# Kernel optimization log

Measured on AMD Instinct MI355X. Metric: run time of the kernel, lower is better.

Reference implementation:

```python
import jax, jax.numpy as jnp
import numpy as np
import math

V = 200000      # num_symbols (pad idx = V)
D = 256         # embed_dim
B = 2048        # query batch
F = 5           # support (few-shot) size
N = 64          # max neighbors per entity
K = 32          # knn_k top-k neighbors kept by cosine sim
DM = 2 * D      # d_model of support/query encoders (512)
HID = 2 * DM    # LSTMCell hidden (1024)
STEPS = 4       # process_steps


def setup_inputs() -> dict:
    key = jax.random.key(0)
    ks = jax.random.split(key, 32)
    xav = lambda k, shp: jax.random.normal(k, shp, jnp.float32) * math.sqrt(2.0 / (shp[0] + shp[1]))
    u = 1.0 / math.sqrt(HID)
    inp = {
        # forward args (int indices)
        "query": jax.random.randint(ks[0], (B, 2), 0, V),
        "support": jax.random.randint(ks[1], (F, 2), 0, V),
        "q_l_conn": jax.random.randint(ks[2], (B, N, 2), 0, V),
        "q_l_deg": jax.random.randint(ks[3], (B,), 1, N),
        "q_r_conn": jax.random.randint(ks[4], (B, N, 2), 0, V),
        "q_r_deg": jax.random.randint(ks[5], (B,), 1, N),
        "s_l_conn": jax.random.randint(ks[6], (F, N, 2), 0, V),
        "s_l_deg": jax.random.randint(ks[7], (F,), 1, N),
        "s_r_conn": jax.random.randint(ks[8], (F, N, 2), 0, V),
        "s_r_deg": jax.random.randint(ks[9], (F,), 1, N),
        # learned params
        "emb": (jax.random.normal(ks[10], (V + 1, D), jnp.float32) * 0.02).at[V].set(0.0),
        "gcn_w": xav(ks[11], (D, 2 * D)),
        "gcn_wb": jnp.zeros((D,), jnp.float32),   # Linear bias of gcn_w
        "gcn_b": jnp.zeros((D,), jnp.float32),    # extra gcn_b Parameter
        "p1_w": xav(ks[12], (2 * DM, DM)),
        "p1_b": jnp.zeros((2 * DM,), jnp.float32),
        "p2_w": xav(ks[13], (DM, 2 * DM)),
        "p2_b": jnp.zeros((DM,), jnp.float32),
        "ln_g": jnp.ones((DM,), jnp.float32),
        "ln_b": jnp.zeros((DM,), jnp.float32),
        "w_ih": jax.random.uniform(ks[14], (4 * HID, DM), jnp.float32, -u, u),
        "w_hh": jax.random.uniform(ks[15], (4 * HID, HID), jnp.float32, -u, u),
        "b_ih": jax.random.uniform(ks[16], (4 * HID,), jnp.float32, -u, u),
        "b_hh": jax.random.uniform(ks[17], (4 * HID,), jnp.float32, -u, u),
    }
    return inp


def reference(query, support, q_l_conn, q_l_deg, q_r_conn, q_r_deg,
              s_l_conn, s_l_deg, s_r_conn, s_r_deg,
              emb, gcn_w, gcn_wb, gcn_b, p1_w, p1_b, p2_w, p2_b,
              ln_g, ln_b, w_ih, w_hh, b_ih, b_hh):
    # dropout is eval-mode identity; knn_path=None so the gate branch is dead.
    # degrees are clamped then unused in the torch code (mean over neighbor dim).
    def neighbor_encoder(conn, ids):
        rel = emb[conn[:, :, 0]]            # (b, N, D) gather
        ent = emb[conn[:, :, 1]]            # (b, N, D)
        center = emb[ids][:, None, :]       # (b, 1, D)
        sim = jnp.sum(center * ent, -1) / jnp.maximum(
            jnp.linalg.norm(center, axis=-1) * jnp.linalg.norm(ent, axis=-1), 1e-8)
        _, idx = jax.lax.top_k(sim, K)      # (b, K)
        rel = jnp.take_along_axis(rel, idx[:, :, None], axis=1)
        ent = jnp.take_along_axis(ent, idx[:, :, None], axis=1)
        cat = jnp.concatenate([rel, ent], axis=-1)               # (b, K, 2D)
        h = jnp.einsum('bkf,df->bkd', cat, gcn_w) + gcn_wb + gcn_b
        return jnp.tanh(h.mean(axis=1))                          # (b, D)

    def support_encoder(x):                 # position-wise FFN + residual + LN
        h = jax.nn.relu(x @ p1_w.T + p1_b)
        o = h @ p2_w.T + p2_b + x
        m = o.mean(-1, keepdims=True)
        v = o.var(-1, keepdims=True)
        return (o - m) / jnp.sqrt(v + 1e-5) * ln_g + ln_b

    ql = neighbor_encoder(q_l_conn, query[:, 0])
    qr = neighbor_encoder(q_r_conn, query[:, 1])
    sl = neighbor_encoder(s_l_conn, support[:, 0])
    sr = neighbor_encoder(s_r_conn, support[:, 1])
    query_n = jnp.concatenate([ql, qr], -1)          # (B, DM)
    supp_n = jnp.concatenate([sl, sr], -1)           # (F, DM)

    support_g = support_encoder(supp_n).mean(axis=0, keepdims=True)   # (1, DM)
    query_g = support_encoder(query_n)                                # (B, DM)

    # QueryEncoder: LSTMCell process block with attention-read over support
    h_r = jnp.zeros((query_g.shape[0], 2 * DM), query_g.dtype)
    c = jnp.zeros((query_g.shape[0], HID), query_g.dtype)
    h = query_g
    for _ in range(STEPS):
        gates = query_g @ w_ih.T + b_ih + h_r @ w_hh.T + b_hh
        i, f, g, o = jnp.split(gates, 4, axis=-1)    # torch gate order i,f,g,o
        c = jax.nn.sigmoid(f) * c + jax.nn.sigmoid(i) * jnp.tanh(g)
        hh = jax.nn.sigmoid(o) * jnp.tanh(c)
        h = query_g + hh[:, :DM]
        attn = jax.nn.softmax(h @ support_g.T, axis=1)   # (B, 1)
        r = attn @ support_g                              # (B, DM)
        h_r = jnp.concatenate([h, r], axis=1)

    query_f = h / jnp.maximum(jnp.linalg.norm(h, axis=-1, keepdims=True), 1e-12)
    sg = support_g[0]
    sg = sg / jnp.maximum(jnp.linalg.norm(sg), 1e-12)
    return query_f @ sg                                   # (B,) cosine scores
```

## Files before the change

### kernel.cpp

```cpp
#include <hip/hip_runtime.h>
#include <math.h>


typedef __attribute__((ext_vector_type(8))) short short8;
typedef __attribute__((ext_vector_type(4))) float floatx4;

__device__ inline unsigned short f2bf(float f) {
  union { float f; unsigned int u; } x;
  x.f = f;
  unsigned int r = x.u + 0x7fffu + ((x.u >> 16) & 1u);
  return (unsigned short)(r >> 16);
}
__device__ inline float bf2f(unsigned short u) {
  union { unsigned int i; float f; } x;
  x.i = ((unsigned int)u) << 16;
  return x.f;
}
__device__ inline float frcp(float x) { return __builtin_amdgcn_rcpf(x); }
__device__ inline float sigm_f(float x) { return frcp(1.f + __expf(-x)); }
__device__ inline float tanh_f(float x) {
  return 1.f - 2.f * frcp(1.f + __expf(2.f * x));
}

#if defined(__has_builtin)
#if __has_builtin(__builtin_amdgcn_global_load_lds)
#define HAVE_GLL 1
#endif
#endif
#ifdef HAVE_GLL
__device__ inline void load_lds16(const void* g, void* l) {
  __builtin_amdgcn_global_load_lds(
      (const __attribute__((address_space(1))) unsigned int*)(uintptr_t)g,
      (__attribute__((address_space(3))) unsigned int*)(unsigned int)(uintptr_t)l,
      16, 0, 0);
}
#else
__device__ inline void load_lds16(const void* g, void* l) {
  const int lane = threadIdx.x & 63;
  *(uint4*)((char*)l + lane * 16) = *(const uint4*)g;
}
#endif

__device__ inline float wave_reduce_sum(float v) {
#pragma unroll
  for (int off = 32; off > 0; off >>= 1) v += __shfl_down(v, off, 64);
  return v;
}

__global__ __launch_bounds__(256) void convert_all_kernel(
    const float* __restrict__ w_ih, const float* __restrict__ w_hh,
    const float* __restrict__ p1_w, const float* __restrict__ p2_w,
    const float* __restrict__ gcn_w, const float* __restrict__ b_ih,
    const float* __restrict__ b_hh, unsigned short* __restrict__ wihb,
    unsigned short* __restrict__ whhb, unsigned short* __restrict__ p1b,
    unsigned short* __restrict__ p2b, unsigned short* __restrict__ gcnb,
    float* __restrict__ bcomb) {
  const int p = blockIdx.x * 256 + threadIdx.x;
  if (p < 262144) {
    const int e = p * 4, r = e >> 9, c = e & 511;
    const int orig = ((r >> 4) & 3) * 1024 + ((r >> 6) << 4) + (r & 15);
    float4 v = *(const float4*)(w_ih + (size_t)orig * 512 + c);
    *(ushort4*)(wihb + (size_t)r * 512 + c) =
        make_ushort4(f2bf(v.x), f2bf(v.y), f2bf(v.z), f2bf(v.w));
  } else if (p < 524288) {
    const int e = (p - 262144) * 4, r = e >> 9, c = e & 511;
    const int orig = ((r >> 4) & 3) * 1024 + ((r >> 6) << 4) + (r & 15);
    float4 v = *(const float4*)(w_hh + (size_t)orig * 1024 + c);
    *(ushort4*)(whhb + (size_t)r * 512 + c) =
        make_ushort4(f2bf(v.x), f2bf(v.y), f2bf(v.z), f2bf(v.w));
  } else if (p < 655360) {
    const int e = (p - 524288) * 4;
    float4 v = *(const float4*)(p1_w + e);
    *(ushort4*)(p1b + e) =
        make_ushort4(f2bf(v.x), f2bf(v.y), f2bf(v.z), f2bf(v.w));
  } else if (p < 786432) {
    const int e = (p - 655360) * 4;
    float4 v = *(const float4*)(p2_w + e);
    *(ushort4*)(p2b + e) =
        make_ushort4(f2bf(v.x), f2bf(v.y), f2bf(v.z), f2bf(v.w));
  } else if (p < 819200) {
    const int e = (p - 786432) * 4;
    float4 v = *(const float4*)(gcn_w + e);
    *(ushort4*)(gcnb + e) =
        make_ushort4(f2bf(v.x), f2bf(v.y), f2bf(v.z), f2bf(v.w));
  } else if (p < 819712) {
    const int c = (p - 819200) * 4;
    const int orig = ((c >> 4) & 3) * 1024 + ((c >> 6) << 4) + (c & 15);
    float4 a = *(const float4*)(b_ih + orig);
    float4 b = *(const float4*)(b_hh + orig);
    *(float4*)(bcomb + c) =
        make_float4(a.x + b.x, a.y + b.y, a.z + b.z, a.w + b.w);
  }
}

__global__ __launch_bounds__(256) void neighbor_kernel(
    const int* __restrict__ query, const int* __restrict__ support,
    const int* __restrict__ qlc, const int* __restrict__ qrc,
    const int* __restrict__ slc, const int* __restrict__ src_,
    const float* __restrict__ emb, unsigned short* __restrict__ mc,
    int B, int F) {
  const int r = blockIdx.x;
  const int tid = threadIdx.x;
  const int* conn;
  int id;
  if (r < B) {
    conn = qlc + (size_t)r * 128; id = query[2 * r];
  } else if (r < 2 * B) {
    int b = r - B; conn = qrc + (size_t)b * 128; id = query[2 * b + 1];
  } else if (r < 2 * B + F) {
    int f = r - 2 * B; conn = slc + (size_t)f * 128; id = support[2 * f];
  } else {
    int f = r - 2 * B - F; conn = src_ + (size_t)f * 128; id = support[2 * f + 1];
  }

  __shared__ __align__(16) float cent[256];
  __shared__ __align__(16) float entpart[4 * 256];
  __shared__ float sims[64];
  __shared__ int rel_ids[64];
  __shared__ int ent_ids[64];
  __shared__ short list[32];
  __shared__ float red[4];
  __shared__ float cnorm_s;
  __shared__ unsigned long long selmask_s;

  if (tid < 64) {
    rel_ids[tid] = conn[2 * tid];
    ent_ids[tid] = conn[2 * tid + 1];
  }
  float cv = emb[(size_t)id * 256 + tid];
  cent[tid] = cv;
  float sq = wave_reduce_sum(cv * cv);
  if ((tid & 63) == 0) red[tid >> 6] = sq;
  __syncthreads();
  if (tid == 0) cnorm_s = sqrtf(red[0] + red[1] + red[2] + red[3]);
  __syncthreads();
  const float cn = cnorm_s;

  const int wave = tid >> 6, lane = tid & 63;
  const float4 cv4 = *(const float4*)(cent + lane * 4);
  uint2 ec[16];
#pragma unroll
  for (int t = 0; t < 16; ++t) {
    const int n = wave + 4 * t;
    const float* er = emb + (size_t)ent_ids[n] * 256;
    float4 e = *(const float4*)(er + lane * 4);
    ec[t].x = (unsigned)f2bf(e.x) | ((unsigned)f2bf(e.y) << 16);
    ec[t].y = (unsigned)f2bf(e.z) | ((unsigned)f2bf(e.w) << 16);
    float d = e.x * cv4.x + e.y * cv4.y + e.z * cv4.z + e.w * cv4.w;
    float s2 = e.x * e.x + e.y * e.y + e.z * e.z + e.w * e.w;
#pragma unroll
    for (int off = 32; off > 0; off >>= 1) {
      d += __shfl_down(d, off, 64);
      s2 += __shfl_down(s2, off, 64);
    }
    if (lane == 0) sims[n] = d / fmaxf(cn * sqrtf(s2), 1e-8f);
  }
  __syncthreads();

  if (wave == 0) {
    float my = sims[lane];
    int rank = 0;
#pragma unroll 8
    for (int j = 0; j < 64; ++j) {
      float sj = sims[j];
      rank += (sj > my) || (sj == my && j < lane);
    }
    if (rank < 32) list[rank] = (short)lane;
    unsigned long long m = __ballot(rank < 32);
    if (lane == 0) selmask_s = m;
  }
  __syncthreads();

  const unsigned long long selm = selmask_s;
  float4 pa = make_float4(0.f, 0.f, 0.f, 0.f);
#pragma unroll
  for (int t = 0; t < 16; ++t) {
    const int n = wave + 4 * t;
    if ((selm >> n) & 1ull) {
      pa.x += bf2f((unsigned short)(ec[t].x & 0xffff));
      pa.y += bf2f((unsigned short)(ec[t].x >> 16));
      pa.z += bf2f((unsigned short)(ec[t].y & 0xffff));
      pa.w += bf2f((unsigned short)(ec[t].y >> 16));
    }
  }
  *(float4*)&entpart[wave * 256 + lane * 4] = pa;
  __syncthreads();

  float accR = 0.f;
#pragma unroll 2
  for (int k = 0; k < 32; k += 4) {
    const int n0 = list[k], n1 = list[k + 1], n2 = list[k + 2], n3 = list[k + 3];
    const float* p0 = emb + (size_t)rel_ids[n0] * 256;
    const float* p1 = emb + (size_t)rel_ids[n1] * 256;
    const float* p2 = emb + (size_t)rel_ids[n2] * 256;
    const float* p3 = emb + (size_t)rel_ids[n3] * 256;
    accR += (p0[tid] + p1[tid]) + (p2[tid] + p3[tid]);
  }
  const float accE = entpart[tid] + entpart[256 + tid] + entpart[512 + tid] +
                     entpart[768 + tid];
  mc[(size_t)r * 512 + tid] = f2bf(accR * (1.f / 32.f));
  mc[(size_t)r * 512 + 256 + tid] = f2bf(accE * (1.f / 32.f));
}

__global__ __launch_bounds__(256) void gemm128_kernel(
    const unsigned short* __restrict__ A, int lda,
    const unsigned short* __restrict__ Bm, int ldb,
    float* __restrict__ C, unsigned short* __restrict__ Cbf,
    int M, int N, int K,
    const float* __restrict__ bias1, const float* __restrict__ bias2,
    const float* __restrict__ addmat, int act, int mode,
    float* __restrict__ cbuf, const float* __restrict__ qg,
    float* __restrict__ h, unsigned short* __restrict__ hbf) {
  __shared__ __align__(16) unsigned short As[128 * 32];
  __shared__ __align__(16) unsigned short Bs[128 * 32];
  const int tid = threadIdx.x;
  const int wid = tid >> 6, lane = tid & 63;
  const int quad = lane >> 4, l16 = lane & 15;
  const int wr = (wid >> 1) * 64, wc = (wid & 1) * 64;
  const int row0 = blockIdx.y * 128, col0 = blockIdx.x * 128;

  const int rl = lane >> 2;
  const int q = (lane & 3) ^ ((lane >> 3) & 3);
  const unsigned short* Ap0 = A + (size_t)(row0 + wid * 32 + rl) * lda + q * 8;
  const unsigned short* Ap1 = Ap0 + (size_t)16 * lda;
  const unsigned short* Bp0 = Bm + (size_t)(col0 + wid * 32 + rl) * ldb + q * 8;
  const unsigned short* Bp1 = Bp0 + (size_t)16 * ldb;
  unsigned short* lA0 = &As[(wid * 32) * 32];
  unsigned short* lA1 = &As[(wid * 32 + 16) * 32];
  unsigned short* lB0 = &Bs[(wid * 32) * 32];
  unsigned short* lB1 = &Bs[(wid * 32 + 16) * 32];

  const int pq = quad ^ ((l16 >> 1) & 3);
  const unsigned short* fA = &As[(wr + l16) * 32 + pq * 8];
  const unsigned short* fB = &Bs[(wc + l16) * 32 + pq * 8];

  floatx4 acc[4][4];
#pragma unroll
  for (int i = 0; i < 4; ++i)
#pragma unroll
    for (int j = 0; j < 4; ++j) {
      floatx4 z = {0.f, 0.f, 0.f, 0.f};
      acc[i][j] = z;
    }

  for (int k0 = 0; k0 < K; k0 += 32) {
    load_lds16(Ap0, lA0);
    load_lds16(Ap1, lA1);
    load_lds16(Bp0, lB0);
    load_lds16(Bp1, lB1);
    Ap0 += 32; Ap1 += 32; Bp0 += 32; Bp1 += 32;
    __syncthreads();

    short8 af[4], bfr[4];
#pragma unroll
    for (int i = 0; i < 4; ++i) af[i] = *(const short8*)(fA + i * 16 * 32);
#pragma unroll
    for (int j = 0; j < 4; ++j) bfr[j] = *(const short8*)(fB + j * 16 * 32);
#pragma unroll
    for (int i = 0; i < 4; ++i)
#pragma unroll
      for (int j = 0; j < 4; ++j)
        acc[i][j] = __builtin_amdgcn_mfma_f32_16x16x32_bf16(af[i], bfr[j],
                                                            acc[i][j], 0, 0, 0);
    __syncthreads();
  }

#pragma unroll
  for (int i = 0; i < 4; ++i) {
#pragma unroll
    for (int r = 0; r < 4; ++r) {
      const int row = row0 + wr + i * 16 + quad * 4 + r;
      float vals[4];
#pragma unroll
      for (int j = 0; j < 4; ++j) {
        const int col = col0 + wc + j * 16 + l16;
        float v = acc[i][j][r];
        if (bias1) v += bias1[col];
        if (bias2) v += bias2[col];
        if (addmat) v += addmat[(size_t)row * N + col];
        vals[j] = v;
      }
      if (mode == 0) {
#pragma unroll
        for (int j = 0; j < 4; ++j) {
          const int col = col0 + wc + j * 16 + l16;
          float v = vals[j];
          if (act == 1) v = tanh_f(v);
          else if (act == 2) v = fmaxf(v, 0.f);
          if (C) C[(size_t)row * N + col] = v;
          if (Cbf) Cbf[(size_t)row * N + col] = f2bf(v);
        }
      } else {
        if (mode == 1) {
#pragma unroll
          for (int j = 0; j < 4; ++j)
            C[(size_t)row * N + (col0 + wc + j * 16 + l16)] = vals[j];
        }
        const int n = (((col0 + wc) >> 6) << 4) + l16;
        const float cold = (mode == 1) ? 0.f : cbuf[(size_t)row * 512 + n];
        const float cn =
            sigm_f(vals[1]) * cold + sigm_f(vals[0]) * tanh_f(vals[2]);
        cbuf[(size_t)row * 512 + n] = cn;
        const float hv =
            qg[(size_t)row * 512 + n] + sigm_f(vals[3]) * tanh_f(cn);
        h[(size_t)row * 512 + n] = hv;
        hbf[(size_t)row * 512 + n] = f2bf(hv);
      }
    }
  }
}

__global__ __launch_bounds__(256) void gemm64_kernel(
    const unsigned short* __restrict__ A, int lda,
    const unsigned short* __restrict__ Bm, int ldb,
    float* __restrict__ C, unsigned short* __restrict__ Cbf,
    int M, int N, int K,
    const float* __restrict__ bias1, const float* __restrict__ bias2,
    const float* __restrict__ addmat, int act, int rB, int rF,
    float* __restrict__ snptr) {
  __shared__ __align__(16) unsigned short As[64 * 32];
  __shared__ __align__(16) unsigned short Bs[64 * 32];
  const int tid = threadIdx.x;
  const int wid = tid >> 6, lane = tid & 63;
  const int quad = lane >> 4, l16 = lane & 15;
  const int wr = (wid >> 1) * 32, wc = (wid & 1) * 32;
  const int row0 = blockIdx.y * 64, col0 = blockIdx.x * 64;

  const int half = wid >> 1;
  const int grp = (wid & 1) * 32;
  const int rl = lane >> 2;
  const int q = (lane & 3) ^ ((lane >> 3) & 3);
  const unsigned short* src = half ? Bm : A;
  const int lds = half ? ldb : lda;
  const int r0s = half ? col0 : row0;
  int rg0 = r0s + grp + rl;
  int rg1 = rg0 + 16;
  if (!half) {
    rg0 = min(rg0, M - 1);
    rg1 = min(rg1, M - 1);
  }
  const unsigned short* P0 = src + (size_t)rg0 * lds + q * 8;
  const unsigned short* P1 = src + (size_t)rg1 * lds + q * 8;
  unsigned short* L0 = (half ? Bs : As) + grp * 32;
  unsigned short* L1 = L0 + 16 * 32;

  const int pq = quad ^ ((l16 >> 1) & 3);
  const unsigned short* fA = &As[(wr + l16) * 32 + pq * 8];
  const unsigned short* fB = &Bs[(wc + l16) * 32 + pq * 8];

  floatx4 acc[2][2];
#pragma unroll
  for (int i = 0; i < 2; ++i)
#pragma unroll
    for (int j = 0; j < 2; ++j) {
      floatx4 z = {0.f, 0.f, 0.f, 0.f};
      acc[i][j] = z;
    }

  for (int k0 = 0; k0 < K; k0 += 32) {
    load_lds16(P0, L0);
    load_lds16(P1, L1);
    P0 += 32; P1 += 32;
    __syncthreads();

    short8 af[2], bfr[2];
#pragma unroll
    for (int i = 0; i < 2; ++i) af[i] = *(const short8*)(fA + i * 16 * 32);
#pragma unroll
    for (int j = 0; j < 2; ++j) bfr[j] = *(const short8*)(fB + j * 16 * 32);
#pragma unroll
    for (int i = 0; i < 2; ++i)
#pragma unroll
      for (int j = 0; j < 2; ++j)
        acc[i][j] = __builtin_amdgcn_mfma_f32_16x16x32_bf16(af[i], bfr[j],
                                                            acc[i][j], 0, 0, 0);
    __syncthreads();
  }

#pragma unroll
  for (int i = 0; i < 2; ++i) {
#pragma unroll
    for (int r = 0; r < 4; ++r) {
      const int row = row0 + wr + i * 16 + quad * 4 + r;
      if (row >= M) continue;
#pragma unroll
      for (int j = 0; j < 2; ++j) {
        const int col = col0 + wc + j * 16 + l16;
        float v = acc[i][j][r];
        if (bias1) v += bias1[col];
        if (bias2) v += bias2[col];
        if (addmat) v += addmat[(size_t)row * N + col];
        if (act == 1) v = tanh_f(v);
        else if (act == 2) v = fmaxf(v, 0.f);
        if (snptr) {
          if (row < rB) {
            C[(size_t)row * 512 + col] = v;
            Cbf[(size_t)row * 512 + col] = f2bf(v);
          } else if (row < 2 * rB) {
            C[(size_t)(row - rB) * 512 + 256 + col] = v;
            Cbf[(size_t)(row - rB) * 512 + 256 + col] = f2bf(v);
          } else if (row < 2 * rB + rF) {
            snptr[(size_t)(row - 2 * rB) * 512 + col] = v;
          } else {
            snptr[(size_t)(row - 2 * rB - rF) * 512 + 256 + col] = v;
          }
        } else {
          if (C) C[(size_t)row * N + col] = v;
          if (Cbf) Cbf[(size_t)row * N + col] = f2bf(v);
        }
      }
    }
  }
}

__global__ __launch_bounds__(256) void gemm_nt_kernel(
    const float* __restrict__ A, int lda, const float* __restrict__ B, int ldb,
    float* __restrict__ C, int M, int N, int K,
    const float* __restrict__ bias1, const float* __restrict__ bias2,
    const float* __restrict__ addmat, int act) {
  __shared__ float As[16][65];
  __shared__ float Bs[16][65];
  const int tid = threadIdx.x;
  const int col0 = blockIdx.x * 64;
  const int row0 = blockIdx.y * 64;
  const int tx = tid & 15, ty = tid >> 4;
  const int lr = tid >> 2, lk = (tid & 3) << 2;

  float acc[4][4];
#pragma unroll
  for (int i = 0; i < 4; ++i)
#pragma unroll
    for (int j = 0; j < 4; ++j) acc[i][j] = 0.f;

  const int ar = row0 + lr;
  const bool avalid = ar < M;
  const float* Aptr = A + (size_t)ar * lda + lk;
  const float* Bptr = B + (size_t)(col0 + lr) * ldb + lk;

  for (int k0 = 0; k0 < K; k0 += 16) {
    float4 av = make_float4(0.f, 0.f, 0.f, 0.f);
    if (avalid) av = *(const float4*)(Aptr + k0);
    float4 bv = *(const float4*)(Bptr + k0);
    As[lk + 0][lr] = av.x; As[lk + 1][lr] = av.y;
    As[lk + 2][lr] = av.z; As[lk + 3][lr] = av.w;
    Bs[lk + 0][lr] = bv.x; Bs[lk + 1][lr] = bv.y;
    Bs[lk + 2][lr] = bv.z; Bs[lk + 3][lr] = bv.w;
    __syncthreads();
#pragma unroll
    for (int k = 0; k < 16; ++k) {
      float a0 = As[k][ty * 4 + 0], a1 = As[k][ty * 4 + 1];
      float a2 = As[k][ty * 4 + 2], a3 = As[k][ty * 4 + 3];
      float b0 = Bs[k][tx * 4 + 0], b1 = Bs[k][tx * 4 + 1];
      float b2 = Bs[k][tx * 4 + 2], b3 = Bs[k][tx * 4 + 3];
      acc[0][0] += a0 * b0; acc[0][1] += a0 * b1; acc[0][2] += a0 * b2; acc[0][3] += a0 * b3;
      acc[1][0] += a1 * b0; acc[1][1] += a1 * b1; acc[1][2] += a1 * b2; acc[1][3] += a1 * b3;
      acc[2][0] += a2 * b0; acc[2][1] += a2 * b1; acc[2][2] += a2 * b2; acc[2][3] += a2 * b3;
      acc[3][0] += a3 * b0; acc[3][1] += a3 * b1; acc[3][2] += a3 * b2; acc[3][3] += a3 * b3;
    }
    __syncthreads();
  }

#pragma unroll
  for (int i = 0; i < 4; ++i) {
    const int r = row0 + ty * 4 + i;
    if (r >= M) continue;
#pragma unroll
    for (int j = 0; j < 4; ++j) {
      const int c = col0 + tx * 4 + j;
      float v = acc[i][j];
      if (bias1) v += bias1[c];
      if (bias2) v += bias2[c];
      if (addmat) v += addmat[(size_t)r * N + c];
      if (act == 1) v = tanhf(v);
      else if (act == 2) v = fmaxf(v, 0.f);
      C[(size_t)r * N + c] = v;
    }
  }
}

__global__ __launch_bounds__(256) void ln_kernel(
    const float* __restrict__ X, float* __restrict__ Y,
    unsigned short* __restrict__ Ybf,
    const float* __restrict__ g, const float* __restrict__ bta) {
  const int r = blockIdx.x;
  const int tid = threadIdx.x;
  const float* x = X + (size_t)r * 512;
  float x0 = x[tid], x1 = x[tid + 256];
  __shared__ float red[4];
  float s = wave_reduce_sum(x0 + x1);
  if ((tid & 63) == 0) red[tid >> 6] = s;
  __syncthreads();
  const float mean = (red[0] + red[1] + red[2] + red[3]) * (1.f / 512.f);
  __syncthreads();
  const float d0 = x0 - mean, d1 = x1 - mean;
  float v = wave_reduce_sum(d0 * d0 + d1 * d1);
  if ((tid & 63) == 0) red[tid >> 6] = v;
  __syncthreads();
  const float var = (red[0] + red[1] + red[2] + red[3]) * (1.f / 512.f);
  const float inv = 1.f / sqrtf(var + 1e-5f);
  const float y0 = d0 * inv * g[tid] + bta[tid];
  const float y1 = d1 * inv * g[tid + 256] + bta[tid + 256];
  float* y = Y + (size_t)r * 512;
  y[tid] = y0;
  y[tid + 256] = y1;
  if (Ybf) {
    Ybf[(size_t)r * 512 + tid] = f2bf(y0);
    Ybf[(size_t)r * 512 + tid + 256] = f2bf(y1);
  }
}

__global__ __launch_bounds__(256) void lns_kernel(
    const float* __restrict__ X, const float* __restrict__ g,
    const float* __restrict__ bta, float* __restrict__ sg, int F) {
  const int tid = threadIdx.x;
  __shared__ float red[4];
  float a0 = 0.f, a1 = 0.f;
  for (int f = 0; f < F; ++f) {
    const float* x = X + (size_t)f * 512;
    const float x0 = x[tid], x1 = x[tid + 256];
    float s = wave_reduce_sum(x0 + x1);
    if ((tid & 63) == 0) red[tid >> 6] = s;
    __syncthreads();
    const float mean = (red[0] + red[1] + red[2] + red[3]) * (1.f / 512.f);
    __syncthreads();
    const float d0 = x0 - mean, d1 = x1 - mean;
    float v = wave_reduce_sum(d0 * d0 + d1 * d1);
    if ((tid & 63) == 0) red[tid >> 6] = v;
    __syncthreads();
    const float var = (red[0] + red[1] + red[2] + red[3]) * (1.f / 512.f);
    const float inv = 1.f / sqrtf(var + 1e-5f);
    a0 += d0 * inv * g[tid] + bta[tid];
    a1 += d1 * inv * g[tid + 256] + bta[tid + 256];
    __syncthreads();
  }
  sg[tid] = a0 / (float)F;
  sg[tid + 256] = a1 / (float)F;
}

__global__ __launch_bounds__(256) void cvec_kernel(
    const float* __restrict__ whh, const float* __restrict__ sg,
    float* __restrict__ cv) {
  const int wave = threadIdx.x >> 6, lane = threadIdx.x & 63;
  const int jp = blockIdx.x * 4 + wave;
  const int orig = ((jp >> 4) & 3) * 1024 + ((jp >> 6) << 4) + (jp & 15);
  const float* wr = whh + (size_t)orig * 1024 + 512;
  float s = 0.f;
#pragma unroll
  for (int d = lane; d < 512; d += 64) s += wr[d] * sg[d];
  s = wave_reduce_sum(s);
  if (lane == 0) cv[jp] = s;
}

__global__ __launch_bounds__(256) void final_kernel(
    const float* __restrict__ h, const float* __restrict__ sg,
    float* __restrict__ out) {
  const int b = blockIdx.x, tid = threadIdx.x;
  const float* hr = h + (size_t)b * 512;
  const float h0 = hr[tid], h1 = hr[tid + 256];
  const float s0 = sg[tid], s1 = sg[tid + 256];
  float d = h0 * s0 + h1 * s1;
  float hh = h0 * h0 + h1 * h1;
  float ssq = s0 * s0 + s1 * s1;
  __shared__ float red[3][4];
  d = wave_reduce_sum(d);
  hh = wave_reduce_sum(hh);
  ssq = wave_reduce_sum(ssq);
  if ((tid & 63) == 0) {
    red[0][tid >> 6] = d; red[1][tid >> 6] = hh; red[2][tid >> 6] = ssq;
  }
  __syncthreads();
  if (tid == 0) {
    const float D = red[0][0] + red[0][1] + red[0][2] + red[0][3];
    const float H = red[1][0] + red[1][1] + red[1][2] + red[1][3];
    const float S = red[2][0] + red[2][1] + red[2][2] + red[2][3];
    out[b] = D / (fmaxf(sqrtf(H), 1e-12f) * fmaxf(sqrtf(S), 1e-12f));
  }
}

extern "C" void kernel_launch(void* const* d_in, const int* in_sizes, int n_in,
                              void* d_out, int out_size, void* d_ws, size_t ws_size,
                              hipStream_t stream) {
  const int* query = (const int*)d_in[0];
  const int* support = (const int*)d_in[1];
  const int* qlc = (const int*)d_in[2];
  const int* qrc = (const int*)d_in[4];
  const int* slc = (const int*)d_in[6];
  const int* src_ = (const int*)d_in[8];
  const float* emb = (const float*)d_in[10];
  const float* gcn_w = (const float*)d_in[11];
  const float* gcn_wb = (const float*)d_in[12];
  const float* gcn_b = (const float*)d_in[13];
  const float* p1_w = (const float*)d_in[14];
  const float* p1_b = (const float*)d_in[15];
  const float* p2_w = (const float*)d_in[16];
  const float* p2_b = (const float*)d_in[17];
  const float* ln_g = (const float*)d_in[18];
  const float* ln_b = (const float*)d_in[19];
  const float* w_ih = (const float*)d_in[20];
  const float* w_hh = (const float*)d_in[21];
  const float* b_ih = (const float*)d_in[22];
  const float* b_hh = (const float*)d_in[23];
  float* out = (float*)d_out;

  const int B = in_sizes[0] / 2;
  const int F = in_sizes[1] / 2;
  const int NR = 2 * B + 2 * F;

  char* Wb = (char*)d_ws;
  size_t off = 0;
  auto alloc = [&](size_t bytes) {
    size_t o = off;
    off += (bytes + 255) & ~(size_t)255;
    return o;
  };
  const size_t base_o = alloc((size_t)B * 2048 * 4);
  const size_t mc_o   = alloc((size_t)NR * 512 * 2);
  const size_t qn_o   = alloc((size_t)B * 512 * 4);
  const size_t qnb_o  = alloc((size_t)B * 512 * 2);
  const size_t hqb_o  = alloc((size_t)B * 1024 * 2);
  const size_t oq_o   = alloc((size_t)B * 512 * 4);
  const size_t qg_o   = alloc((size_t)B * 512 * 4);
  const size_t qgb_o  = alloc((size_t)B * 512 * 2);
  const size_t cbuf_o = alloc((size_t)B * 512 * 4);
  const size_t h_o    = alloc((size_t)B * 512 * 4);
  const size_t hb0_o  = alloc((size_t)B * 512 * 2);
  const size_t hb1_o  = alloc((size_t)B * 512 * 2);
  const size_t wihb_o = alloc((size_t)2048 * 512 * 2);
  const size_t whhb_o = alloc((size_t)2048 * 512 * 2);
  const size_t p1b_o  = alloc((size_t)1024 * 512 * 2);
  const size_t p2b_o  = alloc((size_t)512 * 1024 * 2);
  const size_t gcnb_o = alloc((size_t)256 * 512 * 2);
  const size_t bcomb_o= alloc(2048 * 4);
  const size_t sn_o   = alloc((size_t)F * 512 * 4);
  const size_t hs_o   = alloc((size_t)F * 1024 * 4);
  const size_t oss_o  = alloc((size_t)F * 512 * 4);
  const size_t sg_o   = alloc(512 * 4);
  const size_t cvec_o = alloc(2048 * 4);

  auto F32 = [&](size_t o) { return (float*)(Wb + o); };
  auto BF = [&](size_t o) { return (unsigned short*)(Wb + o); };

  convert_all_kernel<<<3202, 256, 0, stream>>>(
      w_ih, w_hh, p1_w, p2_w, gcn_w, b_ih, b_hh, BF(wihb_o), BF(whhb_o),
      BF(p1b_o), BF(p2b_o), BF(gcnb_o), F32(bcomb_o));

  neighbor_kernel<<<NR, 256, 0, stream>>>(query, support, qlc, qrc, slc, src_,
                                          emb, BF(mc_o), B, F);
  {
    dim3 g(256 / 64, (NR + 63) / 64);
    gemm64_kernel<<<g, 256, 0, stream>>>(BF(mc_o), 512, BF(gcnb_o), 512,
                                         F32(qn_o), BF(qnb_o), NR, 256, 512,
                                         gcn_wb, gcn_b, nullptr, 1, B, F,
                                         F32(sn_o));
  }
  {
    dim3 g(1024 / 64, B / 64);
    gemm64_kernel<<<g, 256, 0, stream>>>(BF(qnb_o), 512, BF(p1b_o), 512,
                                         nullptr, BF(hqb_o), B, 1024, 512,
                                         p1_b, nullptr, nullptr, 2, 0, 0,
                                         nullptr);
  }
  {
    dim3 g(512 / 64, B / 64);
    gemm64_kernel<<<g, 256, 0, stream>>>(BF(hqb_o), 1024, BF(p2b_o), 1024,
                                         F32(oq_o), nullptr, B, 512, 1024,
                                         p2_b, nullptr, F32(qn_o), 0, 0, 0,
                                         nullptr);
  }
  {
    dim3 g(1024 / 64, 1);
    gemm_nt_kernel<<<g, 256, 0, stream>>>(F32(sn_o), 512, p1_w, 512, F32(hs_o),
                                          F, 1024, 512, p1_b, nullptr, nullptr,
                                          2);
  }
  {
    dim3 g(512 / 64, 1);
    gemm_nt_kernel<<<g, 256, 0, stream>>>(F32(hs_o), 1024, p2_w, 1024,
                                          F32(oss_o), F, 512, 1024, p2_b,
                                          nullptr, F32(sn_o), 0);
  }
  lns_kernel<<<1, 256, 0, stream>>>(F32(oss_o), ln_g, ln_b, F32(sg_o), F);
  ln_kernel<<<B, 256, 0, stream>>>(F32(oq_o), F32(qg_o), BF(qgb_o), ln_g, ln_b);
  cvec_kernel<<<512, 256, 0, stream>>>(w_hh, F32(sg_o), F32(cvec_o));
  {
    dim3 g(2048 / 128, B / 128);
    gemm128_kernel<<<g, 256, 0, stream>>>(
        BF(qgb_o), 512, BF(wihb_o), 512, F32(base_o), nullptr, B, 2048, 512,
        F32(bcomb_o), nullptr, nullptr, 0, 1, F32(cbuf_o), F32(qg_o), F32(h_o),
        BF(hb0_o));
  }
  for (int s = 1; s < 4; ++s) {
    const size_t in_o = (s & 1) ? hb0_o : hb1_o;
    const size_t out_o = (s & 1) ? hb1_o : hb0_o;
    dim3 g(2048 / 128, B / 128);
    gemm128_kernel<<<g, 256, 0, stream>>>(
        BF(in_o), 512, BF(whhb_o), 512, nullptr, nullptr, B, 2048, 512,
        F32(cvec_o), nullptr, F32(base_o), 0, 2, F32(cbuf_o), F32(qg_o),
        F32(h_o), BF(out_o));
  }
  final_kernel<<<B, 256, 0, stream>>>(F32(h_o), F32(sg_o), out);
}
```

Before: 725.1 us.

## Fuse four LSTM step GEMMs into one persistent kernel with grid barriers

Replaces the four separate gemm128 launches for the LSTM steps with a single persistent kernel of 256 blocks that loops over the steps and synchronises with a software grid barrier on an atomic counter. The input-projection gates and the cell state now stay in registers across steps instead of being written to and re-read from global base and cell buffers. This removes the per-step global round trips for the base matrix and c, plus three launches. The cost is higher register pressure, and it relies on all 256 blocks being co-resident, since a spinning barrier deadlocks otherwise.

```diff
diff --git a/kernel.cpp b/kernel.cpp
--- a/kernel.cpp
+++ b/kernel.cpp
@@ -47,6 +47,28 @@
   return v;
 }
 
+__device__ inline void grid_barrier(unsigned int* bar, unsigned int nbm1) {
+  __threadfence();
+  __syncthreads();
+  if (threadIdx.x == 0) {
+    unsigned int g =
+        __hip_atomic_load(&bar[1], __ATOMIC_RELAXED, __HIP_MEMORY_SCOPE_AGENT);
+    unsigned int a = __hip_atomic_fetch_add(&bar[0], 1u, __ATOMIC_ACQ_REL,
+                                            __HIP_MEMORY_SCOPE_AGENT);
+    if (a == nbm1) {
+      __hip_atomic_store(&bar[0], 0u, __ATOMIC_RELAXED,
+                         __HIP_MEMORY_SCOPE_AGENT);
+      __hip_atomic_fetch_add(&bar[1], 1u, __ATOMIC_RELEASE,
+                             __HIP_MEMORY_SCOPE_AGENT);
+    } else {
+      while (__hip_atomic_load(&bar[1], __ATOMIC_ACQUIRE,
+                               __HIP_MEMORY_SCOPE_AGENT) == g)
+        __builtin_amdgcn_s_sleep(2);
+    }
+  }
+  __syncthreads();
+}
+
 __global__ __launch_bounds__(256) void convert_all_kernel(
     const float* __restrict__ w_ih, const float* __restrict__ w_hh,
     const float* __restrict__ p1_w, const float* __restrict__ p2_w,
@@ -54,8 +76,9 @@
     const float* __restrict__ b_hh, unsigned short* __restrict__ wihb,
     unsigned short* __restrict__ whhb, unsigned short* __restrict__ p1b,
     unsigned short* __restrict__ p2b, unsigned short* __restrict__ gcnb,
-    float* __restrict__ bcomb) {
+    float* __restrict__ bcomb, unsigned int* __restrict__ bar) {
   const int p = blockIdx.x * 256 + threadIdx.x;
+  if (p == 0) { bar[0] = 0u; bar[1] = 0u; }
   if (p < 262144) {
     const int e = p * 4, r = e >> 9, c = e & 511;
     const int orig = ((r >> 4) & 3) * 1024 + ((r >> 6) << 4) + (r & 15);
@@ -202,15 +225,14 @@
   mc[(size_t)r * 512 + 256 + tid] = f2bf(accE * (1.f / 32.f));
 }
 
-__global__ __launch_bounds__(256) void gemm128_kernel(
-    const unsigned short* __restrict__ A, int lda,
-    const unsigned short* __restrict__ Bm, int ldb,
-    float* __restrict__ C, unsigned short* __restrict__ Cbf,
-    int M, int N, int K,
-    const float* __restrict__ bias1, const float* __restrict__ bias2,
-    const float* __restrict__ addmat, int act, int mode,
-    float* __restrict__ cbuf, const float* __restrict__ qg,
-    float* __restrict__ h, unsigned short* __restrict__ hbf) {
+__global__ __launch_bounds__(256, 1) void lstm_tail_kernel(
+    const unsigned short* __restrict__ qgb,
+    const unsigned short* __restrict__ wihb,
+    const unsigned short* __restrict__ whhb,
+    const float* __restrict__ bcomb, const float* __restrict__ cvec,
+    const float* __restrict__ qg, unsigned short* __restrict__ hb0,
+    unsigned short* __restrict__ hb1, float* __restrict__ hout,
+    unsigned int* __restrict__ bar) {
   __shared__ __align__(16) unsigned short As[128 * 32];
   __shared__ __align__(16) unsigned short Bs[128 * 32];
   const int tid = threadIdx.x;
@@ -218,95 +240,109 @@
   const int quad = lane >> 4, l16 = lane & 15;
   const int wr = (wid >> 1) * 64, wc = (wid & 1) * 64;
   const int row0 = blockIdx.y * 128, col0 = blockIdx.x * 128;
+  const unsigned int nbm1 = gridDim.x * gridDim.y - 1;
 
   const int rl = lane >> 2;
   const int q = (lane & 3) ^ ((lane >> 3) & 3);
-  const unsigned short* Ap0 = A + (size_t)(row0 + wid * 32 + rl) * lda + q * 8;
-  const unsigned short* Ap1 = Ap0 + (size_t)16 * lda;
-  const unsigned short* Bp0 = Bm + (size_t)(col0 + wid * 32 + rl) * ldb + q * 8;
-  const unsigned short* Bp1 = Bp0 + (size_t)16 * ldb;
   unsigned short* lA0 = &As[(wid * 32) * 32];
   unsigned short* lA1 = &As[(wid * 32 + 16) * 32];
   unsigned short* lB0 = &Bs[(wid * 32) * 32];
   unsigned short* lB1 = &Bs[(wid * 32 + 16) * 32];
-
   const int pq = quad ^ ((l16 >> 1) & 3);
   const unsigned short* fA = &As[(wr + l16) * 32 + pq * 8];
   const unsigned short* fB = &Bs[(wc + l16) * 32 + pq * 8];
 
-  floatx4 acc[4][4];
+  const int n = (((col0 + wc) >> 6) << 4) + l16;
+  float bcv[4], cvv[4];
+#pragma unroll
+  for (int j = 0; j < 4; ++j) {
+    const int col = col0 + wc + j * 16 + l16;
+    bcv[j] = bcomb[col];
+    cvv[j] = cvec[col];
+  }
+  float qv[4][4];
 #pragma unroll
   for (int i = 0; i < 4; ++i)
 #pragma unroll
-    for (int j = 0; j < 4; ++j) {
-      floatx4 z = {0.f, 0.f, 0.f, 0.f};
-      acc[i][j] = z;
-    }
-
-  for (int k0 = 0; k0 < K; k0 += 32) {
-    load_lds16(Ap0, lA0);
-    load_lds16(Ap1, lA1);
-    load_lds16(Bp0, lB0);
-    load_lds16(Bp1, lB1);
-    Ap0 += 32; Ap1 += 32; Bp0 += 32; Bp1 += 32;
-    __syncthreads();
-
-    short8 af[4], bfr[4];
-#pragma unroll
-    for (int i = 0; i < 4; ++i) af[i] = *(const short8*)(fA + i * 16 * 32);
-#pragma unroll
-    for (int j = 0; j < 4; ++j) bfr[j] = *(const short8*)(fB + j * 16 * 32);
+    for (int r = 0; r < 4; ++r)
+      qv[i][r] = qg[(size_t)(row0 + wr + i * 16 + quad * 4 + r) * 512 + n];
+
+  float bg[4][4][4];
+  float cb[4][4];
+
+  for (int s = 0; s < 4; ++s) {
+    const unsigned short* Ab = (s == 0) ? qgb : ((s == 2) ? hb1 : hb0);
+    const unsigned short* Bb = (s == 0) ? wihb : whhb;
+    const unsigned short* Ap0 =
+        Ab + (size_t)(row0 + wid * 32 + rl) * 512 + q * 8;
+    const unsigned short* Ap1 = Ap0 + (size_t)16 * 512;
+    const unsigned short* Bp0 =
+        Bb + (size_t)(col0 + wid * 32 + rl) * 512 + q * 8;
+    const unsigned short* Bp1 = Bp0 + (size_t)16 * 512;
+
+    floatx4 acc[4][4];
 #pragma unroll
     for (int i = 0; i < 4; ++i)
 #pragma unroll
-      for (int j = 0; j < 4; ++j)
-        acc[i][j] = __builtin_amdgcn_mfma_f32_16x16x32_bf16(af[i], bfr[j],
-                                                            acc[i][j], 0, 0, 0);
-    __syncthreads();
-  }
-
-#pragma unroll
-  for (int i = 0; i < 4; ++i) {
-#pragma unroll
-    for (int r = 0; r < 4; ++r) {
-      const int row = row0 + wr + i * 16 + quad * 4 + r;
-      float vals[4];
-#pragma unroll
       for (int j = 0; j < 4; ++j) {
-        const int col = col0 + wc + j * 16 + l16;
-        float v = acc[i][j][r];
-        if (bias1) v += bias1[col];
-        if (bias2) v += bias2[col];
-        if (addmat) v += addmat[(size_t)row * N + col];
-        vals[j] = v;
+        floatx4 z = {0.f, 0.f, 0.f, 0.f};
+        acc[i][j] = z;
       }
-      if (mode == 0) {
-#pragma unroll
-        for (int j = 0; j < 4; ++j) {
-          const int col = col0 + wc + j * 16 + l16;
-          float v = vals[j];
-          if (act == 1) v = tanh_f(v);
-          else if (act == 2) v = fmaxf(v, 0.f);
-          if (C) C[(size_t)row * N + col] = v;
-          if (Cbf) Cbf[(size_t)row * N + col] = f2bf(v);
+
+    for (int k0 = 0; k0 < 512; k0 += 32) {
+      load_lds16(Ap0, lA0);
+      load_lds16(Ap1, lA1);
+      load_lds16(Bp0, lB0);
+      load_lds16(Bp1, lB1);
+      Ap0 += 32; Ap1 += 32; Bp0 += 32; Bp1 += 32;
+      __syncthreads();
+
+      short8 af[4], bfr[4];
+#pragma unroll
+      for (int i = 0; i < 4; ++i) af[i] = *(const short8*)(fA + i * 16 * 32);
+#pragma unroll
+      for (int j = 0; j < 4; ++j) bfr[j] = *(const short8*)(fB + j * 16 * 32);
+#pragma unroll
+      for (int i = 0; i < 4; ++i)
+#pragma unroll
+        for (int j = 0; j < 4; ++j)
+          acc[i][j] = __builtin_amdgcn_mfma_f32_16x16x32_bf16(
+              af[i], bfr[j], acc[i][j], 0, 0, 0);
+      __syncthreads();
+    }
+
+    if (s == 0) {
+#pragma unroll
+      for (int i = 0; i < 4; ++i)
+#pragma unroll
+        for (int r = 0; r < 4; ++r) {
+          const int row = row0 + wr + i * 16 + quad * 4 + r;
+#pragma unroll
+          for (int j = 0; j < 4; ++j) bg[i][j][r] = acc[i][j][r] + bcv[j];
+          const float cn = sigm_f(bg[i][0][r]) * tanh_f(bg[i][2][r]);
+          cb[i][r] = cn;
+          const float hv = qv[i][r] + sigm_f(bg[i][3][r]) * tanh_f(cn);
+          hb0[(size_t)row * 512 + n] = f2bf(hv);
         }
-      } else {
-        if (mode == 1) {
-#pragma unroll
-          for (int j = 0; j < 4; ++j)
-            C[(size_t)row * N + (col0 + wc + j * 16 + l16)] = vals[j];
+    } else {
+#pragma unroll
+      for (int i = 0; i < 4; ++i)
+#pragma unroll
+        for (int r = 0; r < 4; ++r) {
+          const int row = row0 + wr + i * 16 + quad * 4 + r;
+          float v0 = acc[i][0][r] + bg[i][0][r] + cvv[0];
+          float v1 = acc[i][1][r] + bg[i][1][r] + cvv[1];
+          float v2 = acc[i][2][r] + bg[i][2][r] + cvv[2];
+          float v3 = acc[i][3][r] + bg[i][3][r] + cvv[3];
+          const float cn = sigm_f(v1) * cb[i][r] + sigm_f(v0) * tanh_f(v2);
+          cb[i][r] = cn;
+          const float hv = qv[i][r] + sigm_f(v3) * tanh_f(cn);
+          if (s == 1) hb1[(size_t)row * 512 + n] = f2bf(hv);
+          else if (s == 2) hb0[(size_t)row * 512 + n] = f2bf(hv);
+          else hout[(size_t)row * 512 + n] = hv;
         }
-        const int n = (((col0 + wc) >> 6) << 4) + l16;
-        const float cold = (mode == 1) ? 0.f : cbuf[(size_t)row * 512 + n];
-        const float cn =
-            sigm_f(vals[1]) * cold + sigm_f(vals[0]) * tanh_f(vals[2]);
-        cbuf[(size_t)row * 512 + n] = cn;
-        const float hv =
-            qg[(size_t)row * 512 + n] + sigm_f(vals[3]) * tanh_f(cn);
-        h[(size_t)row * 512 + n] = hv;
-        hbf[(size_t)row * 512 + n] = f2bf(hv);
-      }
-    }
+    }
+    if (s < 3) grid_barrier(bar, nbm1);
   }
 }
 
@@ -613,7 +649,6 @@
     off += (bytes + 255) & ~(size_t)255;
     return o;
   };
-  const size_t base_o = alloc((size_t)B * 2048 * 4);
   const size_t mc_o   = alloc((size_t)NR * 512 * 2);
   const size_t qn_o   = alloc((size_t)B * 512 * 4);
   const size_t qnb_o  = alloc((size_t)B * 512 * 2);
@@ -621,7 +656,6 @@
   const size_t oq_o   = alloc((size_t)B * 512 * 4);
   const size_t qg_o   = alloc((size_t)B * 512 * 4);
   const size_t qgb_o  = alloc((size_t)B * 512 * 2);
-  const size_t cbuf_o = alloc((size_t)B * 512 * 4);
   const size_t h_o    = alloc((size_t)B * 512 * 4);
   const size_t hb0_o  = alloc((size_t)B * 512 * 2);
   const size_t hb1_o  = alloc((size_t)B * 512 * 2);
@@ -636,13 +670,15 @@
   const size_t oss_o  = alloc((size_t)F * 512 * 4);
   const size_t sg_o   = alloc(512 * 4);
   const size_t cvec_o = alloc(2048 * 4);
+  const size_t bar_o  = alloc(256);
 
   auto F32 = [&](size_t o) { return (float*)(Wb + o); };
   auto BF = [&](size_t o) { return (unsigned short*)(Wb + o); };
 
   convert_all_kernel<<<3202, 256, 0, stream>>>(
       w_ih, w_hh, p1_w, p2_w, gcn_w, b_ih, b_hh, BF(wihb_o), BF(whhb_o),
-      BF(p1b_o), BF(p2b_o), BF(gcnb_o), F32(bcomb_o));
+      BF(p1b_o), BF(p2b_o), BF(gcnb_o), F32(bcomb_o),
+      (unsigned int*)(Wb + bar_o));
 
   neighbor_kernel<<<NR, 256, 0, stream>>>(query, support, qlc, qrc, slc, src_,
                                           emb, BF(mc_o), B, F);
@@ -684,19 +720,10 @@
   cvec_kernel<<<512, 256, 0, stream>>>(w_hh, F32(sg_o), F32(cvec_o));
   {
     dim3 g(2048 / 128, B / 128);
-    gemm128_kernel<<<g, 256, 0, stream>>>(
-        BF(qgb_o), 512, BF(wihb_o), 512, F32(base_o), nullptr, B, 2048, 512,
-        F32(bcomb_o), nullptr, nullptr, 0, 1, F32(cbuf_o), F32(qg_o), F32(h_o),
-        BF(hb0_o));
-  }
-  for (int s = 1; s < 4; ++s) {
-    const size_t in_o = (s & 1) ? hb0_o : hb1_o;
-    const size_t out_o = (s & 1) ? hb1_o : hb0_o;
-    dim3 g(2048 / 128, B / 128);
-    gemm128_kernel<<<g, 256, 0, stream>>>(
-        BF(in_o), 512, BF(whhb_o), 512, nullptr, nullptr, B, 2048, 512,
-        F32(cvec_o), nullptr, F32(base_o), 0, 2, F32(cbuf_o), F32(qg_o),
-        F32(h_o), BF(out_o));
+    lstm_tail_kernel<<<g, 256, 0, stream>>>(
+        BF(qgb_o), BF(wihb_o), BF(whhb_o), F32(bcomb_o), F32(cvec_o),
+        F32(qg_o), BF(hb0_o), BF(hb1_o), F32(h_o),
+        (unsigned int*)(Wb + bar_o));
   }
   final_kernel<<<B, 256, 0, stream>>>(F32(h_o), F32(sg_o), out);
 }
```

Result: slower. 744.3 us (+2.6%).

## Replace LSTM step GEMM with 64x64 double-buffered specialized kernel

Applied to the files above, without the earlier changes.

Replaces the generic 128x128 gemm used for the four LSTM steps with a dedicated 64x64-tile kernel. It double-buffers the LDS loads so the next K-slice loads while MFMAs run, and splits loading so half the waves load A and half load B. The epilogue is specialized, and h is written in fp32 only on the last step and in bf16 only on earlier ones. Smaller tiles quadruple the grid (1024 blocks) to improve CU occupancy at the cost of lower per-block data reuse.

```diff
diff --git a/kernel.cpp b/kernel.cpp
--- a/kernel.cpp
+++ b/kernel.cpp
@@ -202,111 +202,94 @@
   mc[(size_t)r * 512 + 256 + tid] = f2bf(accE * (1.f / 32.f));
 }
 
-__global__ __launch_bounds__(256) void gemm128_kernel(
-    const unsigned short* __restrict__ A, int lda,
-    const unsigned short* __restrict__ Bm, int ldb,
-    float* __restrict__ C, unsigned short* __restrict__ Cbf,
-    int M, int N, int K,
-    const float* __restrict__ bias1, const float* __restrict__ bias2,
-    const float* __restrict__ addmat, int act, int mode,
-    float* __restrict__ cbuf, const float* __restrict__ qg,
-    float* __restrict__ h, unsigned short* __restrict__ hbf) {
-  __shared__ __align__(16) unsigned short As[128 * 32];
-  __shared__ __align__(16) unsigned short Bs[128 * 32];
+__global__ __launch_bounds__(256, 4) void lstm_step_kernel(
+    const unsigned short* __restrict__ A,
+    const unsigned short* __restrict__ Bw,
+    float* __restrict__ base, const float* __restrict__ addvec,
+    const float* __restrict__ qg, float* __restrict__ cbuf,
+    unsigned short* __restrict__ hbf, float* __restrict__ hout, int mode) {
+  __shared__ __align__(16) unsigned short As[2][64 * 32];
+  __shared__ __align__(16) unsigned short Bs[2][64 * 32];
   const int tid = threadIdx.x;
   const int wid = tid >> 6, lane = tid & 63;
   const int quad = lane >> 4, l16 = lane & 15;
-  const int wr = (wid >> 1) * 64, wc = (wid & 1) * 64;
-  const int row0 = blockIdx.y * 128, col0 = blockIdx.x * 128;
-
+  const int row0 = blockIdx.y * 64, col0 = blockIdx.x * 64;
+
+  const int half = wid >> 1;
+  const int grp = (wid & 1) * 32;
   const int rl = lane >> 2;
   const int q = (lane & 3) ^ ((lane >> 3) & 3);
-  const unsigned short* Ap0 = A + (size_t)(row0 + wid * 32 + rl) * lda + q * 8;
-  const unsigned short* Ap1 = Ap0 + (size_t)16 * lda;
-  const unsigned short* Bp0 = Bm + (size_t)(col0 + wid * 32 + rl) * ldb + q * 8;
-  const unsigned short* Bp1 = Bp0 + (size_t)16 * ldb;
-  unsigned short* lA0 = &As[(wid * 32) * 32];
-  unsigned short* lA1 = &As[(wid * 32 + 16) * 32];
-  unsigned short* lB0 = &Bs[(wid * 32) * 32];
-  unsigned short* lB1 = &Bs[(wid * 32 + 16) * 32];
+  const unsigned short* src = half ? Bw : A;
+  const int r0s = half ? col0 : row0;
+  const unsigned short* P0 = src + (size_t)(r0s + grp + rl) * 512 + q * 8;
+  const unsigned short* P1 = P0 + (size_t)16 * 512;
+  const int lofs = grp * 32;
 
   const int pq = quad ^ ((l16 >> 1) & 3);
-  const unsigned short* fA = &As[(wr + l16) * 32 + pq * 8];
-  const unsigned short* fB = &Bs[(wc + l16) * 32 + pq * 8];
-
-  floatx4 acc[4][4];
-#pragma unroll
-  for (int i = 0; i < 4; ++i)
-#pragma unroll
-    for (int j = 0; j < 4; ++j) {
-      floatx4 z = {0.f, 0.f, 0.f, 0.f};
-      acc[i][j] = z;
-    }
-
-  for (int k0 = 0; k0 < K; k0 += 32) {
-    load_lds16(Ap0, lA0);
-    load_lds16(Ap1, lA1);
-    load_lds16(Bp0, lB0);
-    load_lds16(Bp1, lB1);
-    Ap0 += 32; Ap1 += 32; Bp0 += 32; Bp1 += 32;
-    __syncthreads();
-
-    short8 af[4], bfr[4];
-#pragma unroll
-    for (int i = 0; i < 4; ++i) af[i] = *(const short8*)(fA + i * 16 * 32);
-#pragma unroll
-    for (int j = 0; j < 4; ++j) bfr[j] = *(const short8*)(fB + j * 16 * 32);
-#pragma unroll
-    for (int i = 0; i < 4; ++i)
+  const int fAo = (wid * 16 + l16) * 32 + pq * 8;
+  const int fBo = l16 * 32 + pq * 8;
+
+  floatx4 acc[4];
+#pragma unroll
+  for (int j = 0; j < 4; ++j) {
+    floatx4 z = {0.f, 0.f, 0.f, 0.f};
+    acc[j] = z;
+  }
+
+  {
+    unsigned short* L = (half ? Bs[0] : As[0]) + lofs;
+    load_lds16(P0, L);
+    load_lds16(P1, L + 16 * 32);
+    P0 += 32; P1 += 32;
+  }
+  __syncthreads();
+
+  int cur = 0;
+  for (int k0 = 0; k0 < 512; k0 += 32) {
+    if (k0 + 32 < 512) {
+      unsigned short* L = (half ? Bs[cur ^ 1] : As[cur ^ 1]) + lofs;
+      load_lds16(P0, L);
+      load_lds16(P1, L + 16 * 32);
+      P0 += 32; P1 += 32;
+    }
+    const short8 af = *(const short8*)(&As[cur][0] + fAo);
+    short8 bfr[4];
+#pragma unroll
+    for (int j = 0; j < 4; ++j)
+      bfr[j] = *(const short8*)(&Bs[cur][0] + fBo + j * 16 * 32);
+#pragma unroll
+    for (int j = 0; j < 4; ++j)
+      acc[j] = __builtin_amdgcn_mfma_f32_16x16x32_bf16(af, bfr[j], acc[j],
+                                                       0, 0, 0);
+    __syncthreads();
+    cur ^= 1;
+  }
+
+  const int n = ((col0 >> 6) << 4) + l16;
+  float av[4];
+#pragma unroll
+  for (int j = 0; j < 4; ++j) av[j] = addvec[col0 + j * 16 + l16];
+#pragma unroll
+  for (int r = 0; r < 4; ++r) {
+    const int row = row0 + wid * 16 + quad * 4 + r;
+    float v[4];
+#pragma unroll
+    for (int j = 0; j < 4; ++j) v[j] = acc[j][r] + av[j];
+    if (mode == 2) {
 #pragma unroll
       for (int j = 0; j < 4; ++j)
-        acc[i][j] = __builtin_amdgcn_mfma_f32_16x16x32_bf16(af[i], bfr[j],
-                                                            acc[i][j], 0, 0, 0);
-    __syncthreads();
-  }
-
-#pragma unroll
-  for (int i = 0; i < 4; ++i) {
-#pragma unroll
-    for (int r = 0; r < 4; ++r) {
-      const int row = row0 + wr + i * 16 + quad * 4 + r;
-      float vals[4];
-#pragma unroll
-      for (int j = 0; j < 4; ++j) {
-        const int col = col0 + wc + j * 16 + l16;
-        float v = acc[i][j][r];
-        if (bias1) v += bias1[col];
-        if (bias2) v += bias2[col];
-        if (addmat) v += addmat[(size_t)row * N + col];
-        vals[j] = v;
-      }
-      if (mode == 0) {
-#pragma unroll
-        for (int j = 0; j < 4; ++j) {
-          const int col = col0 + wc + j * 16 + l16;
-          float v = vals[j];
-          if (act == 1) v = tanh_f(v);
-          else if (act == 2) v = fmaxf(v, 0.f);
-          if (C) C[(size_t)row * N + col] = v;
-          if (Cbf) Cbf[(size_t)row * N + col] = f2bf(v);
-        }
-      } else {
-        if (mode == 1) {
-#pragma unroll
-          for (int j = 0; j < 4; ++j)
-            C[(size_t)row * N + (col0 + wc + j * 16 + l16)] = vals[j];
-        }
-        const int n = (((col0 + wc) >> 6) << 4) + l16;
-        const float cold = (mode == 1) ? 0.f : cbuf[(size_t)row * 512 + n];
-        const float cn =
-            sigm_f(vals[1]) * cold + sigm_f(vals[0]) * tanh_f(vals[2]);
-        cbuf[(size_t)row * 512 + n] = cn;
-        const float hv =
-            qg[(size_t)row * 512 + n] + sigm_f(vals[3]) * tanh_f(cn);
-        h[(size_t)row * 512 + n] = hv;
-        hbf[(size_t)row * 512 + n] = f2bf(hv);
-      }
-    }
+        v[j] += base[(size_t)row * 2048 + col0 + j * 16 + l16];
+    } else {
+#pragma unroll
+      for (int j = 0; j < 4; ++j)
+        base[(size_t)row * 2048 + col0 + j * 16 + l16] = v[j];
+    }
+    const float cold = (mode == 1) ? 0.f : cbuf[(size_t)row * 512 + n];
+    const float cn = sigm_f(v[1]) * cold + sigm_f(v[0]) * tanh_f(v[2]);
+    cbuf[(size_t)row * 512 + n] = cn;
+    const float hv = qg[(size_t)row * 512 + n] + sigm_f(v[3]) * tanh_f(cn);
+    if (hbf) hbf[(size_t)row * 512 + n] = f2bf(hv);
+    if (hout) hout[(size_t)row * 512 + n] = hv;
   }
 }
 
@@ -683,20 +666,19 @@
   ln_kernel<<<B, 256, 0, stream>>>(F32(oq_o), F32(qg_o), BF(qgb_o), ln_g, ln_b);
   cvec_kernel<<<512, 256, 0, stream>>>(w_hh, F32(sg_o), F32(cvec_o));
   {
-    dim3 g(2048 / 128, B / 128);
-    gemm128_kernel<<<g, 256, 0, stream>>>(
-        BF(qgb_o), 512, BF(wihb_o), 512, F32(base_o), nullptr, B, 2048, 512,
-        F32(bcomb_o), nullptr, nullptr, 0, 1, F32(cbuf_o), F32(qg_o), F32(h_o),
-        BF(hb0_o));
-  }
-  for (int s = 1; s < 4; ++s) {
-    const size_t in_o = (s & 1) ? hb0_o : hb1_o;
-    const size_t out_o = (s & 1) ? hb1_o : hb0_o;
-    dim3 g(2048 / 128, B / 128);
-    gemm128_kernel<<<g, 256, 0, stream>>>(
-        BF(in_o), 512, BF(whhb_o), 512, nullptr, nullptr, B, 2048, 512,
-        F32(cvec_o), nullptr, F32(base_o), 0, 2, F32(cbuf_o), F32(qg_o),
-        F32(h_o), BF(out_o));
+    dim3 g(2048 / 64, B / 64);
+    lstm_step_kernel<<<g, 256, 0, stream>>>(
+        BF(qgb_o), BF(wihb_o), F32(base_o), F32(bcomb_o), F32(qg_o),
+        F32(cbuf_o), BF(hb0_o), nullptr, 1);
+    lstm_step_kernel<<<g, 256, 0, stream>>>(
+        BF(hb0_o), BF(whhb_o), F32(base_o), F32(cvec_o), F32(qg_o),
+        F32(cbuf_o), BF(hb1_o), nullptr, 2);
+    lstm_step_kernel<<<g, 256, 0, stream>>>(
+        BF(hb1_o), BF(whhb_o), F32(base_o), F32(cvec_o), F32(qg_o),
+        F32(cbuf_o), BF(hb0_o), nullptr, 2);
+    lstm_step_kernel<<<g, 256, 0, stream>>>(
+        BF(hb0_o), BF(whhb_o), F32(base_o), F32(cvec_o), F32(qg_o),
+        F32(cbuf_o), nullptr, F32(h_o), 2);
   }
   final_kernel<<<B, 256, 0, stream>>>(F32(h_o), F32(sg_o), out);
 }
```

New measurement: 616.9 us. 1.18x faster.
